# Kernel optimization log

Measured on AMD Instinct MI355X. Metric: run time of the kernel, lower is better.

The kernel has to match this reference:

```python
import jax, jax.numpy as jnp
import numpy as np

HEADS = 8
DIM_HEAD = 64
SCALE = DIM_HEAD ** -0.5

def setup_inputs() -> dict:
    key = jax.random.key(0)
    k1, k2, k3 = jax.random.split(key, 3)
    B, N, D = 4, 2048, 512
    inner = HEADS * DIM_HEAD  # 512
    x = jax.random.normal(k1, (B, N, D), dtype=jnp.float32)
    w_qkv = jax.random.normal(k2, (D, inner * 3), dtype=jnp.float32) * (D ** -0.5)
    w_out = jax.random.normal(k3, (inner, D), dtype=jnp.float32) * (inner ** -0.5)
    b_out = jnp.zeros((D,), dtype=jnp.float32)
    return {"x": x, "w_qkv": w_qkv, "w_out": w_out, "b_out": b_out}

def reference(x, w_qkv, w_out, b_out):
    B, N, D = x.shape
    qkv = x @ w_qkv  # [B, N, 3*inner]
    q, k, v = jnp.split(qkv, 3, axis=-1)
    # b n (h d) -> b h n d
    def to_heads(t):
        return t.reshape(B, N, HEADS, DIM_HEAD).transpose(0, 2, 1, 3)
    q, k, v = to_heads(q), to_heads(k), to_heads(v)
    dots = jnp.einsum('bhid,bhjd->bhij', q, k) * SCALE  # [B,H,N,N]
    attn = jax.nn.softmax(dots, axis=-1)
    out = jnp.einsum('bhij,bhjd->bhid', attn, v)  # [B,H,N,Dh]
    out = out.transpose(0, 2, 1, 3).reshape(B, N, HEADS * DIM_HEAD)
    return out @ w_out + b_out
```

## Files before the change

### kernel.cpp

```cpp
#include <hip/hip_runtime.h>
#include <hip/hip_bf16.h>
#include <math.h>
#include <stdint.h>


typedef unsigned short u16;
typedef __attribute__((ext_vector_type(4))) float f32x4;
typedef __attribute__((ext_vector_type(8))) short bf16x8;
typedef __attribute__((ext_vector_type(4))) short s16x4;

#define AS1 __attribute__((address_space(1)))
#define AS3 __attribute__((address_space(3)))
#define MFMA(a, b, c) __builtin_amdgcn_mfma_f32_16x16x32_bf16(a, b, c, 0, 0, 0)
#define QSCALE 0.180336880f

__device__ __forceinline__ u16 f2bf(float f) {
  union { float f; unsigned u; } v; v.f = f;
  unsigned r = v.u + 0x7FFFu + ((v.u >> 16) & 1u);
  return (u16)(r >> 16);
}
__device__ __forceinline__ float bf2f(u16 b) {
  union { unsigned u; float f; } v; v.u = ((unsigned)b) << 16; return v.f;
}
__device__ __forceinline__ void gld16(const u16* g, u16* l) {
  __builtin_amdgcn_global_load_lds((const AS1 void*)g, (AS3 void*)l, 16, 0, 0);
}
__device__ __forceinline__ float u2f(unsigned u) {
  union { unsigned u; float f; } v; v.u = u; return v.f;
}
__device__ __forceinline__ unsigned f2u(float f) {
  union { float f; unsigned u; } v; v.f = f; return v.u;
}
__device__ __forceinline__ int cvtpk(float lo, float hi) {
  int r; asm("v_cvt_pk_bf16_f32 %0, %1, %2" : "=v"(r) : "v"(lo), "v"(hi));
  return r;
}
__device__ __forceinline__ float fexp2(float x) {
  float r; asm("v_exp_f32 %0, %1" : "=v"(r) : "v"(x));
  return r;
}

__global__ __launch_bounds__(256) void k_prep(
    const float* __restrict__ x,    u16* __restrict__ xh,
    const float* __restrict__ wqkv, u16* __restrict__ wqh,
    const float* __restrict__ wout, u16* __restrict__ woh) {
  const int bid = blockIdx.x, tid = threadIdx.x;
  if (bid < 4096) {
    int i = (bid * 256 + tid) * 4;
    f32x4 v = *(const f32x4*)&x[i];
    s16x4 hh;
    #pragma unroll
    for (int j = 0; j < 4; ++j) hh[j] = (short)f2bf(v[j]);
    *(s16x4*)&xh[i] = hh;
    return;
  }
  __shared__ u16 lds[64][66];
  const float* src; u16* dst; int N, n0, k0;
  if (bid < 4288) {
    const int b2 = bid - 4096;
    src = wqkv; dst = wqh; N = 1536;
    n0 = (b2 % 24) * 64; k0 = (b2 / 24) * 64;
  } else {
    const int b3 = bid - 4288;
    src = wout; dst = woh; N = 512;
    n0 = (b3 & 7) * 64; k0 = (b3 >> 3) * 64;
  }
  const int c = tid & 63, q = tid >> 6;
  #pragma unroll
  for (int s = 0; s < 16; ++s) {
    const int kr = q * 16 + s;
    lds[c][kr] = f2bf(src[(size_t)(k0 + kr) * N + n0 + c]);
  }
  __syncthreads();
  #pragma unroll
  for (int s = 0; s < 16; ++s) {
    const int nr = q * 16 + s;
    dst[(size_t)(n0 + nr) * 512 + k0 + c] = lds[nr][c];
  }
}

__device__ __forceinline__ void gemm_core(
    const u16* __restrict__ Ah, const u16* __restrict__ Bh,
    char* sm, int rowA, int rowB, int tid, f32x4 (&acc)[4][4]) {
  const int wid = tid >> 6, lane = tid & 63;
  const int x = lane & 15, h = lane >> 4;
  const int wr = wid >> 1, wc = wid & 1;
  const int d0 = tid * 16;
  const int lg0 = d0 ^ (((d0 >> 7) & 7) << 4);
  const int srow = lg0 >> 6;
  const int scol = (lg0 & 63) >> 1;
  const int swk = ((lane >> 1) & 7) << 4;
  const int rdoA = ((wr * 64 + x) * 64 + h * 16) ^ swk;
  const int rdoB = (((wc * 64 + x) * 64 + h * 16) ^ swk) + 8192;

  {
    #pragma unroll
    for (int r = 0; r < 2; ++r) {
      const size_t ga = (size_t)(rowA + r * 64 + srow) * 512 + scol;
      const size_t gb = (size_t)(rowB + r * 64 + srow) * 512 + scol;
      gld16(Ah + ga, (u16*)(sm + r * 4096 + d0));
      gld16(Bh + gb, (u16*)(sm + 8192 + r * 4096 + d0));
    }
  }

  for (int kt = 0; kt < 16; ++kt) {
    const int bb = (kt & 1) * 16384;
    __builtin_amdgcn_s_barrier();
    if (kt < 15) {
      const int kofs = (kt + 1) * 32;
      char* buf = sm + (16384 - bb);
      #pragma unroll
      for (int r = 0; r < 2; ++r) {
        const size_t ga = (size_t)(rowA + r * 64 + srow) * 512 + kofs + scol;
        const size_t gb = (size_t)(rowB + r * 64 + srow) * 512 + kofs + scol;
        gld16(Ah + ga, (u16*)(buf + r * 4096 + d0));
        gld16(Bh + gb, (u16*)(buf + 8192 + r * 4096 + d0));
      }
      asm volatile("s_waitcnt vmcnt(4)" ::: "memory");
    } else {
      asm volatile("s_waitcnt vmcnt(0)" ::: "memory");
    }
    __builtin_amdgcn_s_barrier();

    bf16x8 a_h[4], b_h[4];
    #pragma unroll
    for (int i = 0; i < 4; ++i)
      a_h[i] = *(const bf16x8*)(sm + bb + rdoA + i * 1024);
    #pragma unroll
    for (int j = 0; j < 4; ++j)
      b_h[j] = *(const bf16x8*)(sm + bb + rdoB + j * 1024);
    __builtin_amdgcn_s_setprio(1);
    #pragma unroll
    for (int i = 0; i < 4; ++i)
      #pragma unroll
      for (int j = 0; j < 4; ++j)
        acc[i][j] = MFMA(a_h[i], b_h[j], acc[i][j]);
    __builtin_amdgcn_s_setprio(0);
  }
}

__global__ __launch_bounds__(256) void k_gemm_qkv(
    const u16* __restrict__ Ah, const u16* __restrict__ Bh,
    u16* __restrict__ Qb, u16* __restrict__ Kb, u16* __restrict__ Vt) {
  __shared__ __align__(1024) char sm[32768];
  const int tid = threadIdx.x, lane = tid & 63, wid = tid >> 6;
  const int x = lane & 15, h = lane >> 4;
  const int wr = wid >> 1, wc = wid & 1;
  const int rowA = blockIdx.x * 128, rowB = blockIdx.y * 128;
  f32x4 acc[4][4] = {};
  gemm_core(Ah, Bh, sm, rowA, rowB, tid, acc);

  #pragma unroll
  for (int i = 0; i < 4; ++i)
    #pragma unroll
    for (int j = 0; j < 4; ++j) {
      const int n = rowB + wc * 64 + j * 16 + x;
      const int which = n >> 9;
      const int hh = (n >> 6) & 7, d = n & 63;
      const int m0 = rowA + wr * 64 + i * 16 + h * 4;
      const int b = m0 >> 11, is0 = m0 & 2047;
      if (which == 0) {
        #pragma unroll
        for (int r = 0; r < 4; ++r) {
          const size_t idx = ((size_t)((b * 8 + hh) * 2048 + is0 + r)) * 64 + d;
          Qb[idx] = f2bf(acc[i][j][r] * QSCALE);
        }
      } else if (which == 1) {
        #pragma unroll
        for (int r = 0; r < 4; ++r) {
          const size_t idx = ((size_t)((b * 8 + hh) * 2048 + is0 + r)) * 64 + d;
          Kb[idx] = f2bf(acc[i][j][r]);
        }
      } else {
        s16x4 vv;
        #pragma unroll
        for (int r = 0; r < 4; ++r) vv[r] = (short)f2bf(acc[i][j][r]);
        *(s16x4*)&Vt[((size_t)((b * 8 + hh) * 64 + d)) * 2048 + is0] = vv;
      }
    }
}

__global__ __launch_bounds__(256) void k_gemm_out(
    const u16* __restrict__ OP, const float* __restrict__ Mm,
    const float* __restrict__ Sm, const u16* __restrict__ Bh,
    const float* __restrict__ bias, float* __restrict__ out) {
  __shared__ __align__(1024) char sm[32768];
  const int tid = threadIdx.x, lane = tid & 63, wid = tid >> 6;
  const int x = lane & 15, h = lane >> 4;
  const int wr = wid >> 1, wc = wid & 1;
  const int rowA = blockIdx.x * 128, rowB = blockIdx.y * 128;

  const int d0 = tid * 16;
  const int lg0 = d0 ^ (((d0 >> 7) & 7) << 4);
  const int srow = lg0 >> 6;
  const int scol = (lg0 & 63) >> 1;
  const int swk = ((lane >> 1) & 7) << 4;
  const int rdoA = ((wr * 64 + x) * 64 + h * 16) ^ swk;
  const int rdoB = (((wc * 64 + x) * 64 + h * 16) ^ swk) + 8192;

  int bseq[2], srw[2];
  #pragma unroll
  for (int r = 0; r < 2; ++r) {
    const int m = rowA + r * 64 + srow;
    bseq[r] = (m >> 11) * 8;
    srw[r] = m & 2047;
  }

  float w1p[2][8], w2p[2][8];
  #pragma unroll
  for (int r = 0; r < 2; ++r)
    #pragma unroll
    for (int hd = 0; hd < 8; ++hd) {
      const int rb = (bseq[r] + hd) * 2048 + srw[r];
      const float m1 = Mm[rb], m2 = Mm[65536 + rb];
      const float s1 = Sm[rb], s2 = Sm[65536 + rb];
      const float mm = fmaxf(m1, m2);
      const float a1 = fexp2(m1 - mm), a2 = fexp2(m2 - mm);
      const float inv = 1.0f / (s1 * a1 + s2 * a2);
      w1p[r][hd] = a1 * inv; w2p[r][hd] = a2 * inv;
    }

  f32x4 acc[4][4] = {};

  auto stageA = [&](int kt, char* buf) {
    const int head = kt >> 1;
    const int dd = (kt & 1) * 32 + scol;
    #pragma unroll
    for (int r = 0; r < 2; ++r) {
      const int rb = (bseq[r] + head) * 2048 + srw[r];
      const float w1 = w1p[r][head], w2 = w2p[r][head];
      bf16x8 p1 = *(const bf16x8*)&OP[(size_t)rb * 64 + dd];
      bf16x8 p2 = *(const bf16x8*)&OP[4194304 + (size_t)rb * 64 + dd];
      union { int w[4]; bf16x8 v; } uu;
      #pragma unroll
      for (int q = 0; q < 4; ++q) {
        float lo = bf2f((u16)p1[2 * q]) * w1 + bf2f((u16)p2[2 * q]) * w2;
        float hi = bf2f((u16)p1[2 * q + 1]) * w1 + bf2f((u16)p2[2 * q + 1]) * w2;
        uu.w[q] = cvtpk(lo, hi);
      }
      *(bf16x8*)(buf + r * 4096 + d0) = uu.v;
    }
  };

  {
    stageA(0, sm);
    #pragma unroll
    for (int r = 0; r < 2; ++r) {
      const size_t gb = (size_t)(rowB + r * 64 + srow) * 512 + scol;
      gld16(Bh + gb, (u16*)(sm + 8192 + r * 4096 + d0));
    }
    asm volatile("s_waitcnt lgkmcnt(0)" ::: "memory");
    __builtin_amdgcn_sched_barrier(0);
  }

  #pragma unroll
  for (int kt = 0; kt < 16; ++kt) {
    const int bb = (kt & 1) * 16384;
    asm volatile("s_barrier" ::: "memory");
    if (kt < 15) {
      char* buf = sm + (16384 - bb);
      const int kofs = (kt + 1) * 32;
      #pragma unroll
      for (int r = 0; r < 2; ++r) {
        const size_t gb = (size_t)(rowB + r * 64 + srow) * 512 + kofs + scol;
        gld16(Bh + gb, (u16*)(buf + 8192 + r * 4096 + d0));
      }
      stageA(kt + 1, buf);
      asm volatile("s_waitcnt vmcnt(2)" ::: "memory");
      asm volatile("s_waitcnt lgkmcnt(0)" ::: "memory");
      __builtin_amdgcn_sched_barrier(0);
    } else {
      asm volatile("s_waitcnt vmcnt(0)" ::: "memory");
    }
    asm volatile("s_barrier" ::: "memory");

    bf16x8 a_h[4], b_h[4];
    #pragma unroll
    for (int i = 0; i < 4; ++i)
      a_h[i] = *(const bf16x8*)(sm + bb + rdoA + i * 1024);
    #pragma unroll
    for (int j = 0; j < 4; ++j)
      b_h[j] = *(const bf16x8*)(sm + bb + rdoB + j * 1024);
    __builtin_amdgcn_s_setprio(1);
    #pragma unroll
    for (int i = 0; i < 4; ++i)
      #pragma unroll
      for (int j = 0; j < 4; ++j)
        acc[i][j] = MFMA(a_h[i], b_h[j], acc[i][j]);
    __builtin_amdgcn_s_setprio(0);
  }

  #pragma unroll
  for (int i = 0; i < 4; ++i)
    #pragma unroll
    for (int j = 0; j < 4; ++j) {
      const int n = rowB + wc * 64 + j * 16 + x;
      #pragma unroll
      for (int r = 0; r < 4; ++r) {
        const int m = rowA + wr * 64 + i * 16 + h * 4 + r;
        out[(size_t)m * 512 + n] = acc[i][j][r] + bias[n];
      }
    }
}

__global__ __launch_bounds__(512, 2) void k_attn(
    const u16* __restrict__ Qb,
    const u16* __restrict__ Kb, const u16* __restrict__ Vt,
    u16* __restrict__ OP,
    float* __restrict__ Mm,
    float* __restrict__ Sm) {
  __shared__ __align__(1024) char sm[65536];
  const int tid = threadIdx.x, wid = tid >> 6, lane = tid & 63;
  const int x = lane & 15, h = lane >> 4;

  const int fid = blockIdx.x;
  const int l = (fid & 7) * 64 + (fid >> 3);
  const int half = l & 1, qb = (l >> 1) & 7, bh = l >> 4;

  const size_t base = (size_t)bh * 2048 * 64;
  const int qr0 = qb * 256 + wid * 32;
  const size_t kv0 = (size_t)half * 1024;

  bf16x8 qh[2][2];
  #pragma unroll
  for (int g = 0; g < 2; ++g) {
    const size_t rq = base + (size_t)(qr0 + g * 16 + x) * 64 + h * 8;
    #pragma unroll
    for (int ks = 0; ks < 2; ++ks)
      qh[g][ks] = *(const bf16x8*)&Qb[rq + ks * 32];
  }

  bf16x8 ones;
  #pragma unroll
  for (int j = 0; j < 8; ++j) ones[j] = (short)0x3F80;

  const int db = tid * 16;
  const int lg = db ^ (((db >> 7) & 7) << 4);
  const int sks  = db >> 12;
  const int srow = (lg >> 6) & 63;
  const int scb  = (lg & 63) >> 1;
  const size_t offK = (size_t)srow * 64 + sks * 32 + scb;
  const size_t offV = (size_t)srow * 2048 + sks * 32 + scb;

  const int swk = ((lane >> 1) & 7) << 4;
  const int rdo = (x * 64 + h * 16) ^ swk;
  char* const pb = sm + 32768 + wid * 4096;
  const int pxor = (x & 7) << 4;
  const int prow = x * 128;

  float mrun[2] = {-INFINITY, -INFINITY};
  f32x4 o[2][4] = {};
  f32x4 os[2] = {};

  {
    gld16(Kb + base + kv0 * 64 + offK, (u16*)(sm + db));
    gld16(Vt + base + kv0 + offV,      (u16*)(sm + 8192 + db));
  }

  for (int kv = 0; kv < 16; ++kv) {
    const int bb = (kv & 1) * 16384;
    __builtin_amdgcn_s_barrier();
    if (kv < 15) {
      const size_t kvb = kv0 + (size_t)(kv + 1) * 64;
      char* buf = sm + (16384 - bb);
      gld16(Kb + base + kvb * 64 + offK, (u16*)(buf + db));
      gld16(Vt + base + kvb + offV,      (u16*)(buf + 8192 + db));
      asm volatile("s_waitcnt vmcnt(2)" ::: "memory");
    } else {
      asm volatile("s_waitcnt vmcnt(0)" ::: "memory");
    }
    __builtin_amdgcn_s_barrier();

    const char* smb = sm + bb + rdo;

    f32x4 s[2][4] = {};
    __builtin_amdgcn_s_setprio(1);
    #pragma unroll
    for (int c = 0; c < 4; ++c)
      #pragma unroll
      for (int ks = 0; ks < 2; ++ks) {
        bf16x8 kb_ = *(const bf16x8*)(smb + ks * 4096 + c * 1024);
        s[0][c] = MFMA(kb_, qh[0][ks], s[0][c]);
        s[1][c] = MFMA(kb_, qh[1][ks], s[1][c]);
      }
    __builtin_amdgcn_s_setprio(0);

    float pm[2];
    #pragma unroll
    for (int g = 0; g < 2; ++g) {
      float m0 = fmaxf(fmaxf(s[g][0][0], s[g][0][1]), s[g][0][2]);
      float m1 = fmaxf(fmaxf(s[g][0][3], s[g][1][0]), s[g][1][1]);
      float m2 = fmaxf(fmaxf(s[g][1][2], s[g][1][3]), s[g][2][0]);
      float m3 = fmaxf(fmaxf(s[g][2][1], s[g][2][2]), s[g][2][3]);
      float m4 = fmaxf(fmaxf(s[g][3][0], s[g][3][1]), s[g][3][2]);
      float m5 = fmaxf(fmaxf(m0, m1), m2);
      float p  = fmaxf(fmaxf(fmaxf(m3, m4), s[g][3][3]), m5);
      p = fmaxf(p, __shfl_xor(p, 16, 64));
      p = fmaxf(p, __shfl_xor(p, 32, 64));
      pm[g] = p;
    }

    if (__any((pm[0] > mrun[0] + 7.0f) || (pm[1] > mrun[1] + 7.0f))) {
      #pragma unroll
      for (int g = 0; g < 2; ++g) {
        float mnew = fmaxf(mrun[g], pm[g]);
        float scl = fexp2(mrun[g] - mnew);
        mrun[g] = mnew;
        #pragma unroll
        for (int r = 0; r < 4; ++r) {
          float sq = u2f((unsigned)__builtin_amdgcn_ds_bpermute(
              (20 * h + r) * 4, (int)f2u(scl)));
          os[g][r] *= sq;
          #pragma unroll
          for (int dg = 0; dg < 4; ++dg) o[g][dg][r] *= sq;
        }
      }
    }

    #pragma unroll
    for (int g = 0; g < 2; ++g)
      #pragma unroll
      for (int c = 0; c < 4; ++c) {
        int w0 = cvtpk(fexp2(s[g][c][0] - mrun[g]),
                       fexp2(s[g][c][1] - mrun[g]));
        int w1 = cvtpk(fexp2(s[g][c][2] - mrun[g]),
                       fexp2(s[g][c][3] - mrun[g]));
        int* dst = (int*)(pb + g * 2048 + prow + ((c * 32 + h * 8) ^ pxor));
        dst[0] = w0; dst[1] = w1;
      }

    __builtin_amdgcn_s_setprio(1);
    #pragma unroll
    for (int ch = 0; ch < 2; ++ch) {
      bf16x8 pa0 = *(const bf16x8*)(pb + prow +
                                    ((ch * 64 + h * 16) ^ pxor));
      bf16x8 pa1 = *(const bf16x8*)(pb + 2048 + prow +
                                    ((ch * 64 + h * 16) ^ pxor));
      os[0] = MFMA(pa0, ones, os[0]);
      os[1] = MFMA(pa1, ones, os[1]);
      #pragma unroll
      for (int dg = 0; dg < 4; ++dg) {
        bf16x8 vb = *(const bf16x8*)(smb + 8192 + ch * 4096 + dg * 1024);
        o[0][dg] = MFMA(pa0, vb, o[0][dg]);
        o[1][dg] = MFMA(pa1, vb, o[1][dg]);
      }
    }
    __builtin_amdgcn_s_setprio(0);
  }

  u16* op = OP + (size_t)half * 4194304 + ((size_t)(bh * 2048 + qr0)) * 64;
  #pragma unroll
  for (int g = 0; g < 2; ++g) {
    #pragma unroll
    for (int r = 0; r < 4; ++r) {
      const int row = g * 16 + h * 4 + r;
      #pragma unroll
      for (int dg = 0; dg < 4; ++dg)
        op[(size_t)row * 64 + dg * 16 + x] = f2bf(o[g][dg][r]);
      if (x == 0)
        Sm[half * 65536 + bh * 2048 + qr0 + g * 16 + h * 4 + r] = os[g][r];
    }
    if (h == 0)
      Mm[half * 65536 + bh * 2048 + qr0 + g * 16 + x] = mrun[g];
  }
}

extern "C" void kernel_launch(void* const* d_in, const int* in_sizes, int n_in,
                              void* d_out, int out_size, void* d_ws, size_t ws_size,
                              hipStream_t stream) {
  const float* x    = (const float*)d_in[0];
  const float* wqkv = (const float*)d_in[1];
  const float* wout = (const float*)d_in[2];
  const float* bout = (const float*)d_in[3];
  float* out = (float*)d_out;

  char* w = (char*)d_ws;
  u16* xh  = (u16*)(w + 0);
  u16* wqh = (u16*)(w + 16777216);
  u16* woh = (u16*)(w + 19922944);
  u16* Qb  = (u16*)(w + 20971520);
  u16* Kb  = (u16*)(w + 37748736);
  u16* Vt  = (u16*)(w + 46137344);
  u16*   OP = (u16*)(w + 0);
  float* Mm = (float*)(w + 16777216);
  float* Sm = (float*)(w + 17301504);

  k_prep<<<4352, 256, 0, stream>>>(x, xh, wqkv, wqh, wout, woh);
  k_gemm_qkv<<<dim3(64, 12), 256, 0, stream>>>(xh, wqh, Qb, Kb, Vt);
  k_attn<<<512, 512, 0, stream>>>(Qb, Kb, Vt, OP, Mm, Sm);
  k_gemm_out<<<dim3(64, 4), 256, 0, stream>>>(OP, Mm, Sm, woh, bout, out);
}
```

Measured before the change: 93.17 us.

## Fuse fp32-to-bf16 conversion of x into QKV GEMM A-tile staging

Drops the separate x conversion pass from the prep kernel. The QKV GEMM now loads fp32 x directly, packs it to bf16 in registers and writes it to LDS, while B still uses direct global-to-LDS loads. This removes a full write and re-read of the bf16 x buffer in exchange for reading fp32 x (twice the bytes) twelve times, once per N-tile. It also splits the out-GEMM A staging into separate load and write steps so the global loads are issued before the B loads.

```diff
diff --git a/kernel.cpp b/kernel.cpp
--- a/kernel.cpp
+++ b/kernel.cpp
@@ -41,27 +41,16 @@
 }
 
 __global__ __launch_bounds__(256) void k_prep(
-    const float* __restrict__ x,    u16* __restrict__ xh,
     const float* __restrict__ wqkv, u16* __restrict__ wqh,
     const float* __restrict__ wout, u16* __restrict__ woh) {
   const int bid = blockIdx.x, tid = threadIdx.x;
-  if (bid < 4096) {
-    int i = (bid * 256 + tid) * 4;
-    f32x4 v = *(const f32x4*)&x[i];
-    s16x4 hh;
-    #pragma unroll
-    for (int j = 0; j < 4; ++j) hh[j] = (short)f2bf(v[j]);
-    *(s16x4*)&xh[i] = hh;
-    return;
-  }
   __shared__ u16 lds[64][66];
   const float* src; u16* dst; int N, n0, k0;
-  if (bid < 4288) {
-    const int b2 = bid - 4096;
+  if (bid < 192) {
     src = wqkv; dst = wqh; N = 1536;
-    n0 = (b2 % 24) * 64; k0 = (b2 / 24) * 64;
+    n0 = (bid % 24) * 64; k0 = (bid / 24) * 64;
   } else {
-    const int b3 = bid - 4288;
+    const int b3 = bid - 192;
     src = wout; dst = woh; N = 512;
     n0 = (b3 & 7) * 64; k0 = (b3 >> 3) * 64;
   }
@@ -79,12 +68,15 @@
   }
 }
 
-__device__ __forceinline__ void gemm_core(
-    const u16* __restrict__ Ah, const u16* __restrict__ Bh,
-    char* sm, int rowA, int rowB, int tid, f32x4 (&acc)[4][4]) {
-  const int wid = tid >> 6, lane = tid & 63;
+__global__ __launch_bounds__(256) void k_gemm_qkv(
+    const float* __restrict__ xf, const u16* __restrict__ Bh,
+    u16* __restrict__ Qb, u16* __restrict__ Kb, u16* __restrict__ Vt) {
+  __shared__ __align__(1024) char sm[32768];
+  const int tid = threadIdx.x, lane = tid & 63, wid = tid >> 6;
   const int x = lane & 15, h = lane >> 4;
   const int wr = wid >> 1, wc = wid & 1;
+  const int rowA = blockIdx.x * 128, rowB = blockIdx.y * 128;
+
   const int d0 = tid * 16;
   const int lg0 = d0 ^ (((d0 >> 7) & 7) << 4);
   const int srow = lg0 >> 6;
@@ -93,34 +85,69 @@
   const int rdoA = ((wr * 64 + x) * 64 + h * 16) ^ swk;
   const int rdoB = (((wc * 64 + x) * 64 + h * 16) ^ swk) + 8192;
 
+  f32x4 acc[4][4] = {};
+
   {
+    f32x4 a0[2], a1[2];
     #pragma unroll
     for (int r = 0; r < 2; ++r) {
-      const size_t ga = (size_t)(rowA + r * 64 + srow) * 512 + scol;
+      const float* src = xf + (size_t)(rowA + r * 64 + srow) * 512 + scol;
+      a0[r] = *(const f32x4*)src;
+      a1[r] = *(const f32x4*)(src + 4);
+    }
+    #pragma unroll
+    for (int r = 0; r < 2; ++r) {
       const size_t gb = (size_t)(rowB + r * 64 + srow) * 512 + scol;
-      gld16(Ah + ga, (u16*)(sm + r * 4096 + d0));
       gld16(Bh + gb, (u16*)(sm + 8192 + r * 4096 + d0));
     }
+    #pragma unroll
+    for (int r = 0; r < 2; ++r) {
+      union { int w[4]; bf16x8 v; } uu;
+      uu.w[0] = cvtpk(a0[r][0], a0[r][1]);
+      uu.w[1] = cvtpk(a0[r][2], a0[r][3]);
+      uu.w[2] = cvtpk(a1[r][0], a1[r][1]);
+      uu.w[3] = cvtpk(a1[r][2], a1[r][3]);
+      *(bf16x8*)(sm + r * 4096 + d0) = uu.v;
+    }
+    asm volatile("s_waitcnt lgkmcnt(0)" ::: "memory");
+    __builtin_amdgcn_sched_barrier(0);
   }
 
   for (int kt = 0; kt < 16; ++kt) {
     const int bb = (kt & 1) * 16384;
-    __builtin_amdgcn_s_barrier();
+    asm volatile("s_barrier" ::: "memory");
     if (kt < 15) {
+      char* buf = sm + (16384 - bb);
       const int kofs = (kt + 1) * 32;
-      char* buf = sm + (16384 - bb);
+      f32x4 a0[2], a1[2];
       #pragma unroll
       for (int r = 0; r < 2; ++r) {
-        const size_t ga = (size_t)(rowA + r * 64 + srow) * 512 + kofs + scol;
+        const float* src = xf + (size_t)(rowA + r * 64 + srow) * 512 +
+                           kofs + scol;
+        a0[r] = *(const f32x4*)src;
+        a1[r] = *(const f32x4*)(src + 4);
+      }
+      #pragma unroll
+      for (int r = 0; r < 2; ++r) {
         const size_t gb = (size_t)(rowB + r * 64 + srow) * 512 + kofs + scol;
-        gld16(Ah + ga, (u16*)(buf + r * 4096 + d0));
         gld16(Bh + gb, (u16*)(buf + 8192 + r * 4096 + d0));
       }
-      asm volatile("s_waitcnt vmcnt(4)" ::: "memory");
+      #pragma unroll
+      for (int r = 0; r < 2; ++r) {
+        union { int w[4]; bf16x8 v; } uu;
+        uu.w[0] = cvtpk(a0[r][0], a0[r][1]);
+        uu.w[1] = cvtpk(a0[r][2], a0[r][3]);
+        uu.w[2] = cvtpk(a1[r][0], a1[r][1]);
+        uu.w[3] = cvtpk(a1[r][2], a1[r][3]);
+        *(bf16x8*)(buf + r * 4096 + d0) = uu.v;
+      }
+      asm volatile("s_waitcnt vmcnt(2)" ::: "memory");
+      asm volatile("s_waitcnt lgkmcnt(0)" ::: "memory");
+      __builtin_amdgcn_sched_barrier(0);
     } else {
       asm volatile("s_waitcnt vmcnt(0)" ::: "memory");
     }
-    __builtin_amdgcn_s_barrier();
+    asm volatile("s_barrier" ::: "memory");
 
     bf16x8 a_h[4], b_h[4];
     #pragma unroll
@@ -137,18 +164,6 @@
         acc[i][j] = MFMA(a_h[i], b_h[j], acc[i][j]);
     __builtin_amdgcn_s_setprio(0);
   }
-}
-
-__global__ __launch_bounds__(256) void k_gemm_qkv(
-    const u16* __restrict__ Ah, const u16* __restrict__ Bh,
-    u16* __restrict__ Qb, u16* __restrict__ Kb, u16* __restrict__ Vt) {
-  __shared__ __align__(1024) char sm[32768];
-  const int tid = threadIdx.x, lane = tid & 63, wid = tid >> 6;
-  const int x = lane & 15, h = lane >> 4;
-  const int wr = wid >> 1, wc = wid & 1;
-  const int rowA = blockIdx.x * 128, rowB = blockIdx.y * 128;
-  f32x4 acc[4][4] = {};
-  gemm_core(Ah, Bh, sm, rowA, rowB, tid, acc);
 
   #pragma unroll
   for (int i = 0; i < 4; ++i)
@@ -222,20 +237,28 @@
 
   f32x4 acc[4][4] = {};
 
-  auto stageA = [&](int kt, char* buf) {
+  auto loadA = [&](int kt, bf16x8 (&p1)[2], bf16x8 (&p2)[2]) {
     const int head = kt >> 1;
     const int dd = (kt & 1) * 32 + scol;
     #pragma unroll
     for (int r = 0; r < 2; ++r) {
       const int rb = (bseq[r] + head) * 2048 + srw[r];
+      p1[r] = *(const bf16x8*)&OP[(size_t)rb * 64 + dd];
+      p2[r] = *(const bf16x8*)&OP[4194304 + (size_t)rb * 64 + dd];
+    }
+  };
+  auto writeA = [&](int kt, const bf16x8 (&p1)[2], const bf16x8 (&p2)[2],
+                    char* buf) {
+    const int head = kt >> 1;
+    #pragma unroll
+    for (int r = 0; r < 2; ++r) {
       const float w1 = w1p[r][head], w2 = w2p[r][head];
-      bf16x8 p1 = *(const bf16x8*)&OP[(size_t)rb * 64 + dd];
-      bf16x8 p2 = *(const bf16x8*)&OP[4194304 + (size_t)rb * 64 + dd];
       union { int w[4]; bf16x8 v; } uu;
       #pragma unroll
       for (int q = 0; q < 4; ++q) {
-        float lo = bf2f((u16)p1[2 * q]) * w1 + bf2f((u16)p2[2 * q]) * w2;
-        float hi = bf2f((u16)p1[2 * q + 1]) * w1 + bf2f((u16)p2[2 * q + 1]) * w2;
+        float lo = bf2f((u16)p1[r][2 * q]) * w1 + bf2f((u16)p2[r][2 * q]) * w2;
+        float hi = bf2f((u16)p1[r][2 * q + 1]) * w1 +
+                   bf2f((u16)p2[r][2 * q + 1]) * w2;
         uu.w[q] = cvtpk(lo, hi);
       }
       *(bf16x8*)(buf + r * 4096 + d0) = uu.v;
@@ -243,12 +266,14 @@
   };
 
   {
-    stageA(0, sm);
+    bf16x8 p1[2], p2[2];
+    loadA(0, p1, p2);
     #pragma unroll
     for (int r = 0; r < 2; ++r) {
       const size_t gb = (size_t)(rowB + r * 64 + srow) * 512 + scol;
       gld16(Bh + gb, (u16*)(sm + 8192 + r * 4096 + d0));
     }
+    writeA(0, p1, p2, sm);
     asm volatile("s_waitcnt lgkmcnt(0)" ::: "memory");
     __builtin_amdgcn_sched_barrier(0);
   }
@@ -260,12 +285,14 @@
     if (kt < 15) {
       char* buf = sm + (16384 - bb);
       const int kofs = (kt + 1) * 32;
+      bf16x8 p1[2], p2[2];
+      loadA(kt + 1, p1, p2);
       #pragma unroll
       for (int r = 0; r < 2; ++r) {
         const size_t gb = (size_t)(rowB + r * 64 + srow) * 512 + kofs + scol;
         gld16(Bh + gb, (u16*)(buf + 8192 + r * 4096 + d0));
       }
-      stageA(kt + 1, buf);
+      writeA(kt + 1, p1, p2, buf);
       asm volatile("s_waitcnt vmcnt(2)" ::: "memory");
       asm volatile("s_waitcnt lgkmcnt(0)" ::: "memory");
       __builtin_amdgcn_sched_barrier(0);
@@ -475,7 +502,6 @@
   float* out = (float*)d_out;
 
   char* w = (char*)d_ws;
-  u16* xh  = (u16*)(w + 0);
   u16* wqh = (u16*)(w + 16777216);
   u16* woh = (u16*)(w + 19922944);
   u16* Qb  = (u16*)(w + 20971520);
@@ -485,8 +511,8 @@
   float* Mm = (float*)(w + 16777216);
   float* Sm = (float*)(w + 17301504);
 
-  k_prep<<<4352, 256, 0, stream>>>(x, xh, wqkv, wqh, wout, woh);
-  k_gemm_qkv<<<dim3(64, 12), 256, 0, stream>>>(xh, wqh, Qb, Kb, Vt);
+  k_prep<<<256, 256, 0, stream>>>(wqkv, wqh, wout, woh);
+  k_gemm_qkv<<<dim3(64, 12), 256, 0, stream>>>(x, wqh, Qb, Kb, Vt);
   k_attn<<<512, 512, 0, stream>>>(Qb, Kb, Vt, OP, Mm, Sm);
   k_gemm_out<<<dim3(64, 4), 256, 0, stream>>>(OP, Mm, Sm, woh, bout, out);
 }
```

Result: no change. 92.22 us (-1.0%).
